# Kernel optimization log

Measured on AMD Instinct MI355X. Metric: run time of the kernel, lower is better.

## Reference

```python
import jax, jax.numpy as jnp
import numpy as np

N_LAYERS = 4
EPS = 1e-5  # eqx.nn.LayerNorm default


def _kernels(lam, P, B, C, step, L):
    # Annotated-S4 DPLR generating-function kernel (Q = P), vectorized over H channels.
    # lam, P, B, C: (H, N) complex64; step: (H, 1) real. Returns K: (H, L) real.
    omega = jnp.exp((-2j * jnp.pi) * (jnp.arange(L) / L))            # (L,) roots of unity
    g = (2.0 / step) * ((1.0 - omega) / (1.0 + omega))[None, :]      # (H, L) bilinear warp
    c = 2.0 / (1.0 + omega)                                          # (L,)

    def cauchy(v):  # v: (H, N) -> (H, L): sum_n v_n / (g - lambda_n)
        return jnp.sum(v[:, None, :] / (g[:, :, None] - lam[:, None, :]), axis=-1)

    k00 = cauchy(jnp.conj(C) * B)
    k01 = cauchy(jnp.conj(C) * P)
    k10 = cauchy(jnp.conj(P) * B)
    k11 = cauchy(jnp.conj(P) * P)
    at_roots = c[None, :] * (k00 - k01 * (1.0 / (1.0 + k11)) * k10)  # woodbury correction
    return jnp.fft.ifft(at_roots, n=L, axis=-1).real                 # (H, L)


def _causal_conv(u, K):
    # u: (B, L, H) real input, K: (H, L) real kernel -> causal conv along L via zero-padded FFT.
    L = u.shape[1]
    Ud = jnp.fft.rfft(u, n=2 * L, axis=1)                 # (B, F, H)
    Kd = jnp.fft.rfft(K, n=2 * L, axis=-1)                # (H, F)
    return jnp.fft.irfft(Ud * Kd.T[None], n=2 * L, axis=1)[:, :L]


def _forward(x, enc_w, enc_b, dec_w, dec_b, lam_re, lam_im, p_re, p_im, b_re, b_im,
             c_re, c_im, d, log_step, norm_w, norm_b, w1, b1, w2, b2):
    L = x.shape[1]
    h = x @ enc_w.T + enc_b                               # encoder: (B, L, H)
    for i in range(N_LAYERS):
        skip = h
        mu = h.mean(-1, keepdims=True)
        var = ((h - mu) ** 2).mean(-1, keepdims=True)
        hn = (h - mu) / jnp.sqrt(var + EPS) * norm_w[i] + norm_b[i]
        K = _kernels(lam_re[i] + 1j * lam_im[i], p_re[i] + 1j * p_im[i],
                     b_re[i] + 1j * b_im[i], c_re[i] + 1j * c_im[i],
                     jnp.exp(log_step[i])[:, None], L)
        y = _causal_conv(hn, K) + hn * d[i]               # SSM conv + skip-through D term
        y = jax.nn.gelu(y)
        y = (y @ w1[i].T + b1[i]) * jax.nn.sigmoid(y @ w2[i].T + b2[i])  # gated MLP
        h = skip + y
    return h @ dec_w.T + dec_b                            # decoder: (B, L, out)


def setup_inputs() -> dict:
    key = jax.random.key(0)
    B, L, IN, OUT, H, N, NL = 8, 2048, 64, 64, 128, 64, N_LAYERS
    ks = jax.random.split(key, 12)
    rn = lambda k, s, sc: (jax.random.normal(k, s) * sc).astype(jnp.float32)
    return dict(
        x=rn(ks[0], (B, L, IN), 1.0),
        convolve=1,
        enc_w=rn(ks[1], (H, IN), 1.0 / np.sqrt(IN)), enc_b=jnp.zeros((H,), jnp.float32),
        dec_w=rn(ks[2], (OUT, H), 1.0 / np.sqrt(H)), dec_b=jnp.zeros((OUT,), jnp.float32),
        lam_re=-0.5 * jnp.ones((NL, H, N), jnp.float32),  # HiPPO/S4D-style stable poles
        lam_im=jnp.tile(jnp.float32(np.pi) * jnp.arange(N, dtype=jnp.float32), (NL, H, 1)),
        p_re=rn(ks[3], (NL, H, N), 0.5 / np.sqrt(N)), p_im=rn(ks[4], (NL, H, N), 0.5 / np.sqrt(N)),
        b_re=rn(ks[5], (NL, H, N), 1.0), b_im=rn(ks[6], (NL, H, N), 1.0),
        c_re=rn(ks[7], (NL, H, N), 1.0 / np.sqrt(N)), c_im=rn(ks[8], (NL, H, N), 1.0 / np.sqrt(N)),
        d=jnp.ones((NL, H), jnp.float32),
        log_step=(jax.random.uniform(ks[9], (NL, H)) * (np.log(0.1) - np.log(0.001))
                  + np.log(0.001)).astype(jnp.float32),
        norm_w=jnp.ones((NL, H), jnp.float32), norm_b=jnp.zeros((NL, H), jnp.float32),
        w1=rn(ks[10], (NL, H, H), 1.0 / np.sqrt(H)), b1=jnp.zeros((NL, H), jnp.float32),
        w2=rn(ks[11], (NL, H, H), 1.0 / np.sqrt(H)), b2=jnp.zeros((NL, H), jnp.float32),
    )


def reference(x, convolve, enc_w, enc_b, dec_w, dec_b, lam_re, lam_im, p_re, p_im,
              b_re, b_im, c_re, c_im, d, log_step, norm_w, norm_b, w1, b1, w2, b2):
    # convolve is static 1 (True): the FFT-convolution path of the S4 Model.
    return _forward(x, enc_w, enc_b, dec_w, dec_b, lam_re, lam_im, p_re, p_im, b_re, b_im,
                    c_re, c_im, d, log_step, norm_w, norm_b, w1, b1, w2, b2)
```

## Files before the change

### kernel.cpp

```cpp
#include <hip/hip_runtime.h>
#include <hip/hip_bf16.h>


#define Bsz 8
#define Lseq 2048
#define Hdim 128
#define Npol 64
#define NLAYERS 4

typedef __bf16 bf16x8 __attribute__((ext_vector_type(8)));
typedef float f32x16 __attribute__((ext_vector_type(16)));

__device__ __forceinline__ float fast_rcp(float x) { return __builtin_amdgcn_rcpf(x); }
__device__ __forceinline__ float fast_rsq(float x) { return __builtin_amdgcn_rsqf(x); }

__device__ __forceinline__ float2 cmulf(float2 a, float2 b) {
    return make_float2(a.x * b.x - a.y * b.y, a.x * b.y + a.y * b.x);
}
__device__ __forceinline__ float2 cmulc(float2 a, float2 b) {
    return make_float2(a.x * b.x + a.y * b.y, a.y * b.x - a.x * b.y);
}

__device__ __forceinline__ float gelu_f(float v) {
    float z = 0.7978845608028654f * (v + 0.044715f * v * v * v);
    float e = __expf(2.0f * z);
    return v - v * fast_rcp(e + 1.0f);
}

__device__ __forceinline__ int sw(int i) { return (i & ~15) | ((i ^ (i >> 4)) & 15); }

static __device__ const float W16R[8] = {1.f, 0.9238795325f, 0.7071067812f, 0.3826834324f,
                                         0.f, -0.3826834324f, -0.7071067812f, -0.9238795325f};
static __device__ const float W16I[8] = {0.f, -0.3826834324f, -0.7071067812f, -0.9238795325f,
                                         -1.f, -0.9238795325f, -0.7071067812f, -0.3826834324f};
static __device__ const int BR4[16] = {0, 8, 4, 12, 2, 10, 6, 14, 1, 9, 5, 13, 3, 11, 7, 15};
static __device__ const int BR3[8] = {0, 4, 2, 6, 1, 5, 3, 7};

__device__ __forceinline__ float2 twget(const float2* __restrict__ tw, int e) {
    float2 w = tw[e & 2047];
    if (e & 2048) { w.x = -w.x; w.y = -w.y; }
    return w;
}

template <bool INV>
__device__ __forceinline__ void fft16_dif(float2 v[16]) {
#pragma unroll
    for (int mi = 0; mi < 4; mi++) {
        const int m = 8 >> mi;
#pragma unroll
        for (int g = 0; g < 16; g += 2 * m) {
#pragma unroll
            for (int j = 0; j < m; j++) {
                float wr = W16R[j << mi];
                float wi = INV ? -W16I[j << mi] : W16I[j << mi];
                float2 a = v[g + j], b = v[g + j + m];
                float dx = a.x - b.x, dy = a.y - b.y;
                v[g + j] = make_float2(a.x + b.x, a.y + b.y);
                v[g + j + m] = make_float2(dx * wr - dy * wi, dx * wi + dy * wr);
            }
        }
    }
}

template <bool INV>
__device__ __forceinline__ void fft16_dit(float2 v[16]) {
#pragma unroll
    for (int mi = 3; mi >= 0; mi--) {
        const int m = 8 >> mi;
#pragma unroll
        for (int g = 0; g < 16; g += 2 * m) {
#pragma unroll
            for (int j = 0; j < m; j++) {
                float wr = W16R[j << mi];
                float wi = INV ? -W16I[j << mi] : W16I[j << mi];
                float2 a = v[g + j], b = v[g + j + m];
                float bx = b.x * wr - b.y * wi, by = b.x * wi + b.y * wr;
                v[g + j] = make_float2(a.x + bx, a.y + by);
                v[g + j + m] = make_float2(a.x - bx, a.y - by);
            }
        }
    }
}

template <bool INV>
__device__ __forceinline__ void fft8_dif(float2 v[8]) {
#pragma unroll
    for (int mi = 0; mi < 3; mi++) {
        const int m = 4 >> mi;
#pragma unroll
        for (int g = 0; g < 8; g += 2 * m) {
#pragma unroll
            for (int j = 0; j < m; j++) {
                float wr = W16R[j << (mi + 1)];
                float wi = INV ? -W16I[j << (mi + 1)] : W16I[j << (mi + 1)];
                float2 a = v[g + j], b = v[g + j + m];
                float dx = a.x - b.x, dy = a.y - b.y;
                v[g + j] = make_float2(a.x + b.x, a.y + b.y);
                v[g + j + m] = make_float2(dx * wr - dy * wi, dx * wi + dy * wr);
            }
        }
    }
}

__device__ __forceinline__ void fft4096_passA_hz(float2* data, const float2* __restrict__ tw,
                                                 int t, const float2 vin[8]) {
    float2 v[16];
#pragma unroll
    for (int j = 0; j < 8; j++) v[j] = vin[j];
#pragma unroll
    for (int j = 0; j < 8; j++)
        v[j + 8] = cmulf(v[j], make_float2(W16R[j], W16I[j]));
#pragma unroll
    for (int mi = 1; mi < 4; mi++) {
        const int m = 8 >> mi;
#pragma unroll
        for (int g = 0; g < 16; g += 2 * m) {
#pragma unroll
            for (int j = 0; j < m; j++) {
                float wr = W16R[j << mi], wi = W16I[j << mi];
                float2 a = v[g + j], b = v[g + j + m];
                float dx = a.x - b.x, dy = a.y - b.y;
                v[g + j] = make_float2(a.x + b.x, a.y + b.y);
                v[g + j + m] = make_float2(dx * wr - dy * wi, dx * wi + dy * wr);
            }
        }
    }
#pragma unroll
    for (int i = 1; i < 16; i++) v[i] = cmulf(v[i], twget(tw, t * BR4[i]));
#pragma unroll
    for (int i = 0; i < 16; i++) data[sw(i * 256 + t)] = v[i];
}

__device__ __forceinline__ void fft4096_fwd_BC(float2* data, const float2* __restrict__ tw, int t) {
    __syncthreads();
    {
        int j0 = t & 15;
        int base = (t >> 4) * 256 + j0;
        float2 v[16];
#pragma unroll
        for (int k = 0; k < 16; k++) v[k] = data[sw(base + 16 * k)];
        fft16_dif<false>(v);
#pragma unroll
        for (int i = 1; i < 16; i++) v[i] = cmulf(v[i], twget(tw, 16 * j0 * BR4[i]));
#pragma unroll
        for (int i = 0; i < 16; i++) data[sw(base + 16 * i)] = v[i];
    }
    __syncthreads();
    {
        float2 v[16];
#pragma unroll
        for (int k = 0; k < 16; k++) v[k] = data[sw(t * 16 + k)];
        fft16_dif<false>(v);
#pragma unroll
        for (int i = 0; i < 16; i++) data[sw(t * 16 + i)] = v[i];
    }
    __syncthreads();
}

__global__ __launch_bounds__(256, 4) void prep_kernel(const float* __restrict__ w1,
                                                      const float* __restrict__ w2,
                                                      const float* __restrict__ dec_w,
                                                      float2* __restrict__ tw,
                                                      __bf16* __restrict__ wbf,
                                                      __bf16* __restrict__ decbf) {
    int bid = blockIdx.x, t = threadIdx.x;
    if (bid < 8) {
        int k = bid * 256 + t;
        if (k < 2048) {
            double a = -6.283185307179586476925286766559 * (double)k / 4096.0;
            tw[k] = make_float2((float)cos(a), (float)sin(a));
        }
        return;
    }
    if (bid < 264) {
        int i = (bid - 8) * 256 + t;
        int layer = i >> 14, rem = i & 16383;
        wbf[((size_t)layer * 2) * 16384 + rem] = (__bf16)w1[i];
        wbf[((size_t)layer * 2 + 1) * 16384 + rem] = (__bf16)w2[i];
        return;
    }
    int i = (bid - 264) * 256 + t;
    decbf[i] = (__bf16)dec_w[i];
}

__global__ __launch_bounds__(256) void kfft_enc_kernel(float2* __restrict__ Kd1,
                                                       const float2* __restrict__ tw,
                                                       const float* __restrict__ x,
                                                       const float* __restrict__ enc_w,
                                                       const float* __restrict__ enc_b,
                                                       const float* __restrict__ nw,
                                                       const float* __restrict__ nb,
                                                       float* __restrict__ h,
                                                       float* __restrict__ hnT,
                                                       const float* __restrict__ lam_re,
                                                       const float* __restrict__ lam_im,
                                                       const float* __restrict__ p_re,
                                                       const float* __restrict__ p_im,
                                                       const float* __restrict__ b_re,
                                                       const float* __restrict__ b_im,
                                                       const float* __restrict__ c_re,
                                                       const float* __restrict__ c_im,
                                                       const float* __restrict__ log_step) {
    __shared__ __align__(16) float smem[11712];
    int bid = blockIdx.x, t = threadIdx.x;
    if (bid < 512) {
        int hh = bid & 127, layer = bid >> 7;
        float2* data = (float2*)smem;
        float* ktmp = smem + 8192;
        float4* polA = (float4*)(smem + 10240);
        float4* polB = (float4*)(smem + 10496);
        float* n11S = smem + 10752;
        int baseP = (layer * Hdim + hh) * Npol;
        if (t < Npol) {
            int n = t;
            float lr = lam_re[baseP + n], li = lam_im[baseP + n];
            float pr = p_re[baseP + n], pi = p_im[baseP + n];
            float br = b_re[baseP + n], bi = b_im[baseP + n];
            float cr = c_re[baseP + n], ci = c_im[baseP + n];
            polA[n] = make_float4(lr, li, cr * br + ci * bi, cr * bi - ci * br);
            polB[n] = make_float4(cr * pr + ci * pi, cr * pi - ci * pr,
                                  pr * br + pi * bi, pr * bi - pi * br);
            n11S[n] = pr * pr + pi * pi;
        }
        __syncthreads();
        {
            float step = expf(log_step[layer * Hdim + hh]);
            float gs = 2.0f / step;
            float wrv[8], wiv[8];
            float gr[8], gi[8];
#pragma unroll
            for (int j = 0; j < 8; j++) {
                int l = t + 256 * j;
                float ang = -6.283185307179586f * (float)l / (float)Lseq;
                float wr = cosf(ang), wi = sinf(ang);
                wrv[j] = wr; wiv[j] = wi;
                float dr = 1.0f + wr, di = wi;
                float invd2 = fast_rcp(dr * dr + di * di);
                float nr = 1.0f - wr, ni = -wi;
                gr[j] = gs * (nr * dr + ni * di) * invd2;
                gi[j] = gs * (ni * dr - nr * di) * invd2;
            }
            float k00x[8], k00y[8], k01x[8], k01y[8];
            float k10x[8], k10y[8], k11x[8], k11y[8];
#pragma unroll
            for (int j = 0; j < 8; j++) {
                k00x[j] = 0.f; k00y[j] = 0.f; k01x[j] = 0.f; k01y[j] = 0.f;
                k10x[j] = 0.f; k10y[j] = 0.f; k11x[j] = 0.f; k11y[j] = 0.f;
            }
            for (int n = 0; n < Npol; n++) {
                float4 A = polA[n];
                float4 B = polB[n];
                float n11 = n11S[n];
#pragma unroll
                for (int j = 0; j < 8; j++) {
                    float er = gr[j] - A.x, ei = gi[j] - A.y;
                    float inv2 = fast_rcp(fmaf(er, er, ei * ei));
                    float ir = er * inv2;
                    float mi = ei * inv2;
                    k00x[j] = fmaf(A.z, ir, fmaf(A.w, mi, k00x[j]));
                    k00y[j] = fmaf(A.w, ir, fmaf(-A.z, mi, k00y[j]));
                    k01x[j] = fmaf(B.x, ir, fmaf(B.y, mi, k01x[j]));
                    k01y[j] = fmaf(B.y, ir, fmaf(-B.x, mi, k01y[j]));
                    k10x[j] = fmaf(B.z, ir, fmaf(B.w, mi, k10x[j]));
                    k10y[j] = fmaf(B.w, ir, fmaf(-B.z, mi, k10y[j]));
                    k11x[j] = fmaf(n11, ir, k11x[j]);
                    k11y[j] = fmaf(-n11, mi, k11y[j]);
                }
            }
#pragma unroll
            for (int j = 0; j < 8; j++) {
                int l = t + 256 * j;
                float dr = 1.0f + wrv[j], di = wiv[j];
                float invd2 = fast_rcp(dr * dr + di * di);
                float cr2 = 2.0f * dr * invd2, ci2 = -2.0f * di * invd2;
                float wr2 = 1.0f + k11x[j], wi2 = k11y[j];
                float w2inv = fast_rcp(fmaf(wr2, wr2, wi2 * wi2));
                float vr = wr2 * w2inv, vi = -wi2 * w2inv;
                float t1x = k01x[j] * k10x[j] - k01y[j] * k10y[j];
                float t1y = k01x[j] * k10y[j] + k01y[j] * k10x[j];
                float t2x = t1x * vr - t1y * vi, t2y = t1x * vi + t1y * vr;
                float ex = k00x[j] - t2x, ey = k00y[j] - t2y;
                data[sw(l)] = make_float2(cr2 * ex - ci2 * ey, cr2 * ey + ci2 * ex);
            }
        }
        __syncthreads();
        if (t < 128) {
            float2 v[16];
#pragma unroll
            for (int k = 0; k < 16; k++) v[k] = data[sw(t + 128 * k)];
            fft16_dif<true>(v);
#pragma unroll
            for (int i = 1; i < 16; i++) v[i] = cmulc(v[i], twget(tw, 2 * t * BR4[i]));
#pragma unroll
            for (int i = 0; i < 16; i++) data[sw(i * 128 + t)] = v[i];
        }
        __syncthreads();
        if (t < 128) {
            int i2 = t >> 3, j0 = t & 7;
            int base2 = i2 * 128 + j0;
            float2 v[16];
#pragma unroll
            for (int k = 0; k < 16; k++) v[k] = data[sw(base2 + 8 * k)];
            fft16_dif<true>(v);
#pragma unroll
            for (int i = 1; i < 16; i++) v[i] = cmulc(v[i], twget(tw, 32 * j0 * BR4[i]));
#pragma unroll
            for (int i = 0; i < 16; i++) data[sw(base2 + 8 * i)] = v[i];
        }
        __syncthreads();
        {
            float2 v8[8];
#pragma unroll
            for (int k = 0; k < 8; k++) v8[k] = data[sw(t * 8 + k)];
            fft8_dif<true>(v8);
            int r = BR4[t >> 4], s = BR4[t & 15];
#pragma unroll
            for (int i = 0; i < 8; i++) {
                int l = r + 16 * s + 256 * BR3[i];
                ktmp[l] = v8[i].x * (1.0f / 2048.0f);
            }
        }
        __syncthreads();
        {
            float2 vin[8];
#pragma unroll
            for (int k = 0; k < 8; k++) vin[k] = make_float2(ktmp[t + 256 * k], 0.f);
            fft4096_passA_hz(data, tw, t, vin);
        }
        fft4096_fwd_BC(data, tw, t);
        float2* dst = Kd1 + ((size_t)layer * Hdim + hh) * 4096;
#pragma unroll
        for (int k = 0; k < 16; k++) {
            int p = t + 256 * k;
            dst[p] = data[sw(p)];
        }
    } else {
        int r0 = (bid - 512) * 16;
        float* ws = smem;
        float* xst = smem + 8320;
        float* dots = smem + 9600;
        float2* mv = (float2*)(smem + 11648);
        for (int i = t; i < 128 * 64; i += 256) ws[(i >> 6) * 65 + (i & 63)] = enc_w[i];
        for (int i = t; i < 16 * 64; i += 256) {
            int r = i >> 6, k = i & 63;
            xst[k * 20 + r] = x[(size_t)(r0 + r) * 64 + k];
        }
        __syncthreads();
        int o = t & 127, half = t >> 7;
        float acc[8];
        float bo = enc_b[o];
#pragma unroll
        for (int j = 0; j < 8; j++) acc[j] = bo;
        for (int k = 0; k < 64; k++) {
            float wv = ws[o * 65 + k];
            float4 xa = *(const float4*)&xst[k * 20 + half * 8];
            float4 xb = *(const float4*)&xst[k * 20 + half * 8 + 4];
            acc[0] += wv * xa.x; acc[1] += wv * xa.y; acc[2] += wv * xa.z; acc[3] += wv * xa.w;
            acc[4] += wv * xb.x; acc[5] += wv * xb.y; acc[6] += wv * xb.z; acc[7] += wv * xb.w;
        }
#pragma unroll
        for (int j = 0; j < 8; j++) dots[(half * 8 + j) * 128 + o] = acc[j];
        __syncthreads();
        {
            int row = t >> 4, lane = t & 15;
            float s1 = 0.f, s2 = 0.f;
#pragma unroll
            for (int i = 0; i < 8; i++) {
                float v = dots[row * 128 + lane * 8 + i];
                s1 += v; s2 += v * v;
            }
#pragma unroll
            for (int m = 1; m < 16; m <<= 1) { s1 += __shfl_xor(s1, m); s2 += __shfl_xor(s2, m); }
            if (lane == 0) {
                float mu = s1 * (1.0f / 128.0f);
                float var = s2 * (1.0f / 128.0f) - mu * mu;
                mv[row] = make_float2(mu, fast_rsq(var + 1e-5f));
            }
        }
        __syncthreads();
        int c = t & 127;
        int bb = r0 >> 11, l0 = r0 & 2047;
        float nwc = nw[c], nbc = nb[c];
        float hnv[8];
#pragma unroll
        for (int j = 0; j < 8; j++) {
            int r = half * 8 + j;
            float v = dots[r * 128 + c];
            h[(size_t)(r0 + r) * Hdim + c] = v;
            float2 m = mv[r];
            hnv[j] = (v - m.x) * m.y * nwc + nbc;
        }
        float* dst = hnT + ((size_t)bb * Hdim + c) * Lseq + l0 + half * 8;
        *(float4*)dst = make_float4(hnv[0], hnv[1], hnv[2], hnv[3]);
        *(float4*)(dst + 4) = make_float4(hnv[4], hnv[5], hnv[6], hnv[7]);
    }
}

__global__ __launch_bounds__(256) void conv_kernel(float* __restrict__ hnT,
                                                   const float2* __restrict__ Kd1,
                                                   const float* __restrict__ dvec,
                                                   const float2* __restrict__ tw) {
    int h = blockIdx.x, bp = blockIdx.y, t = threadIdx.x;
    __shared__ float2 data[4096];
    float* u0 = hnT + ((size_t)(2 * bp) * Hdim + h) * Lseq;
    float* u1 = hnT + ((size_t)(2 * bp + 1) * Hdim + h) * Lseq;
    float2 ureg[8];
    float2 Kreg[16];
    float2 twB[15];
    const int j0 = t & 15;
    const float4* Kp4 = (const float4*)(Kd1 + (size_t)h * 4096 + t * 16);
    {
        float2 vin[8];
#pragma unroll
        for (int k = 0; k < 8; k++) {
            int l = t + 256 * k;
            float2 u2 = make_float2(u0[l], u1[l]);
            ureg[k] = u2;
            vin[k] = u2;
        }
#pragma unroll
        for (int k = 0; k < 8; k++) {
            float4 q = Kp4[k];
            Kreg[2 * k]     = make_float2(q.x, q.y);
            Kreg[2 * k + 1] = make_float2(q.z, q.w);
        }
#pragma unroll
        for (int i = 1; i < 16; i++) twB[i - 1] = twget(tw, 16 * j0 * BR4[i]);
        fft4096_passA_hz(data, tw, t, vin);
    }
    __syncthreads();
    {
        int base = (t >> 4) * 256 + j0;
        float2 v[16];
#pragma unroll
        for (int k = 0; k < 16; k++) v[k] = data[sw(base + 16 * k)];
        fft16_dif<false>(v);
#pragma unroll
        for (int i = 1; i < 16; i++) v[i] = cmulf(v[i], twB[i - 1]);
#pragma unroll
        for (int i = 0; i < 16; i++) data[sw(base + 16 * i)] = v[i];
    }
    __syncthreads();
    {
        const float scale = 1.0f / 4096.0f;
        float2 v[16];
#pragma unroll
        for (int k = 0; k < 16; k++) v[k] = data[sw(t * 16 + k)];
        fft16_dif<false>(v);
#pragma unroll
        for (int i = 0; i < 16; i++) {
            float2 W = cmulf(v[i], Kreg[i]);
            v[i] = make_float2(W.x * scale, W.y * scale);
        }
        fft16_dit<true>(v);
#pragma unroll
        for (int i = 0; i < 16; i++) data[sw(t * 16 + i)] = v[i];
    }
    __syncthreads();
    {
        int base2 = (t >> 4) * 256 + j0;
        float2 v[16];
        v[0] = data[sw(base2)];
#pragma unroll
        for (int i = 1; i < 16; i++)
            v[i] = cmulc(data[sw(base2 + 16 * i)], twB[i - 1]);
        fft16_dit<true>(v);
#pragma unroll
        for (int i = 0; i < 16; i++) data[sw(base2 + 16 * i)] = v[i];
    }
    __syncthreads();
    {
        float2 v[16];
        v[0] = data[sw(t)];
#pragma unroll
        for (int i = 1; i < 16; i++)
            v[i] = cmulc(data[sw(i * 256 + t)], twget(tw, t * BR4[i]));
#pragma unroll
        for (int mi = 3; mi >= 1; mi--) {
            const int m = 8 >> mi;
#pragma unroll
            for (int g = 0; g < 16; g += 2 * m) {
#pragma unroll
                for (int j = 0; j < m; j++) {
                    float wr = W16R[j << mi], wi = -W16I[j << mi];
                    float2 a = v[g + j], bb2 = v[g + j + m];
                    float bx = bb2.x * wr - bb2.y * wi, by = bb2.x * wi + bb2.y * wr;
                    v[g + j] = make_float2(a.x + bx, a.y + by);
                    v[g + j + m] = make_float2(a.x - bx, a.y - by);
                }
            }
        }
#pragma unroll
        for (int j = 0; j < 8; j++) {
            float wr = W16R[j], wi = -W16I[j];
            float2 bb2 = v[j + 8];
            float bx = bb2.x * wr - bb2.y * wi, by = bb2.x * wi + bb2.y * wr;
            v[j] = make_float2(v[j].x + bx, v[j].y + by);
        }
        float dcoef = dvec[h];
#pragma unroll
        for (int k = 0; k < 8; k++) {
            int l = t + 256 * k;
            u0[l] = gelu_f(v[k].x + ureg[k].x * dcoef);
            u1[l] = gelu_f(v[k].y + ureg[k].y * dcoef);
        }
    }
}

__global__ __launch_bounds__(256) void mlp_kernel(const float* __restrict__ yT,
                                                  float* __restrict__ h,
                                                  float* __restrict__ hnT,
                                                  const __bf16* __restrict__ w1b,
                                                  const __bf16* __restrict__ w2b,
                                                  const float* __restrict__ b1,
                                                  const float* __restrict__ b2,
                                                  const float* __restrict__ nw,
                                                  const float* __restrict__ nb) {
    int r0 = blockIdx.x * 32;
    int t = threadIdx.x;
    int wave = t >> 6, lane = t & 63;
    __shared__ __align__(16) __bf16 ybf[32 * 136];
    __shared__ float dots[32 * 132];
    __shared__ float2 mv[32];
    int bb = r0 >> 11, l0 = r0 & 2047;
    for (int i = t; i < 32 * 128; i += 256) {
        int r = i & 31, k = i >> 5;
        ybf[r * 136 + k] = (__bf16)yT[((size_t)bb * Hdim + k) * Lseq + l0 + r];
    }
    __syncthreads();
    int m = lane & 31, half = lane >> 5;
    bf16x8 a[8];
#pragma unroll
    for (int kk = 0; kk < 8; kk++)
        a[kk] = *(const bf16x8*)&ybf[m * 136 + kk * 16 + half * 8];
    int out = 32 * wave + m;
    const __bf16* w1r = w1b + (size_t)out * 128 + half * 8;
    const __bf16* w2r = w2b + (size_t)out * 128 + half * 8;
    f32x16 acc1, acc2;
#pragma unroll
    for (int i = 0; i < 16; i++) { acc1[i] = 0.f; acc2[i] = 0.f; }
#pragma unroll
    for (int kk = 0; kk < 8; kk++) {
        bf16x8 bw1 = *(const bf16x8*)(w1r + kk * 16);
        bf16x8 bw2 = *(const bf16x8*)(w2r + kk * 16);
        acc1 = __builtin_amdgcn_mfma_f32_32x32x16_bf16(a[kk], bw1, acc1, 0, 0, 0);
        acc2 = __builtin_amdgcn_mfma_f32_32x32x16_bf16(a[kk], bw2, acc2, 0, 0, 0);
    }
    float bias1 = b1[out], bias2 = b2[out];
#pragma unroll
    for (int reg = 0; reg < 16; reg++) {
        int row = (reg & 3) + 8 * (reg >> 2) + 4 * half;
        float v1 = acc1[reg] + bias1;
        float v2 = acc2[reg] + bias2;
        float g = fast_rcp(1.0f + __expf(-v2));
        float hv = h[(size_t)(r0 + row) * Hdim + out] + v1 * g;
        dots[row * 132 + out] = hv;
    }
    __syncthreads();
    {
        int row = t >> 3, lane8 = t & 7;
        float s1 = 0.f, s2 = 0.f;
        int base = row * 132 + lane8 * 16;
#pragma unroll
        for (int q = 0; q < 4; q++) {
            float4 v4 = *(const float4*)&dots[base + 4 * q];
            s1 += v4.x + v4.y + v4.z + v4.w;
            s2 += v4.x * v4.x + v4.y * v4.y + v4.z * v4.z + v4.w * v4.w;
        }
#pragma unroll
        for (int mm = 1; mm < 8; mm <<= 1) { s1 += __shfl_xor(s1, mm); s2 += __shfl_xor(s2, mm); }
        if (lane8 == 0) {
            float mu = s1 * (1.0f / 128.0f);
            float var = s2 * (1.0f / 128.0f) - mu * mu;
            mv[row] = make_float2(mu, fast_rsq(var + 1e-5f));
        }
    }
    __syncthreads();
    {
        int o = t & 127, rh = t >> 7;
        float nwc = nw[o], nbc = nb[o];
        float hnv[16];
#pragma unroll
        for (int j = 0; j < 16; j++) {
            int r = rh * 16 + j;
            float hvv = dots[r * 132 + o];
            h[(size_t)(r0 + r) * Hdim + o] = hvv;
            float2 mvv = mv[r];
            hnv[j] = (hvv - mvv.x) * mvv.y * nwc + nbc;
        }
        float* dst = hnT + ((size_t)bb * Hdim + o) * Lseq + l0 + rh * 16;
        *(float4*)(dst)      = make_float4(hnv[0],  hnv[1],  hnv[2],  hnv[3]);
        *(float4*)(dst + 4)  = make_float4(hnv[4],  hnv[5],  hnv[6],  hnv[7]);
        *(float4*)(dst + 8)  = make_float4(hnv[8],  hnv[9],  hnv[10], hnv[11]);
        *(float4*)(dst + 12) = make_float4(hnv[12], hnv[13], hnv[14], hnv[15]);
    }
}

__global__ __launch_bounds__(256) void mlpdec_kernel(const float* __restrict__ yT,
                                                     const float* __restrict__ h,
                                                     const __bf16* __restrict__ w1b,
                                                     const __bf16* __restrict__ w2b,
                                                     const float* __restrict__ b1,
                                                     const float* __restrict__ b2,
                                                     const __bf16* __restrict__ decb,
                                                     const float* __restrict__ dec_bias,
                                                     float* __restrict__ out) {
    int r0 = blockIdx.x * 32;
    int t = threadIdx.x;
    int wave = t >> 6, lane = t & 63;
    __shared__ __align__(16) __bf16 ybf[32 * 136];
    __shared__ float dots[32 * 132];
    int bb = r0 >> 11, l0 = r0 & 2047;
    for (int i = t; i < 32 * 128; i += 256) {
        int r = i & 31, k = i >> 5;
        ybf[r * 136 + k] = (__bf16)yT[((size_t)bb * Hdim + k) * Lseq + l0 + r];
    }
    __syncthreads();
    int m = lane & 31, half = lane >> 5;
    bf16x8 a[8];
#pragma unroll
    for (int kk = 0; kk < 8; kk++)
        a[kk] = *(const bf16x8*)&ybf[m * 136 + kk * 16 + half * 8];
    int outc = 32 * wave + m;
    const __bf16* w1r = w1b + (size_t)outc * 128 + half * 8;
    const __bf16* w2r = w2b + (size_t)outc * 128 + half * 8;
    f32x16 acc1, acc2;
#pragma unroll
    for (int i = 0; i < 16; i++) { acc1[i] = 0.f; acc2[i] = 0.f; }
#pragma unroll
    for (int kk = 0; kk < 8; kk++) {
        bf16x8 bw1 = *(const bf16x8*)(w1r + kk * 16);
        bf16x8 bw2 = *(const bf16x8*)(w2r + kk * 16);
        acc1 = __builtin_amdgcn_mfma_f32_32x32x16_bf16(a[kk], bw1, acc1, 0, 0, 0);
        acc2 = __builtin_amdgcn_mfma_f32_32x32x16_bf16(a[kk], bw2, acc2, 0, 0, 0);
    }
    float bias1 = b1[outc], bias2 = b2[outc];
#pragma unroll
    for (int reg = 0; reg < 16; reg++) {
        int row = (reg & 3) + 8 * (reg >> 2) + 4 * half;
        float v1 = acc1[reg] + bias1;
        float v2 = acc2[reg] + bias2;
        float g = fast_rcp(1.0f + __expf(-v2));
        float hv = h[(size_t)(r0 + row) * Hdim + outc] + v1 * g;
        dots[row * 132 + outc] = hv;
    }
    __syncthreads();
    for (int i = t; i < 32 * 128; i += 256) {
        int r = i >> 7, k = i & 127;
        ybf[r * 136 + k] = (__bf16)dots[r * 132 + k];
    }
    __syncthreads();
    if (wave < 2) {
        bf16x8 a2[8];
#pragma unroll
        for (int kk = 0; kk < 8; kk++)
            a2[kk] = *(const bf16x8*)&ybf[m * 136 + kk * 16 + half * 8];
        int oc = 32 * wave + m;
        const __bf16* wr = decb + (size_t)oc * 128 + half * 8;
        f32x16 acc;
#pragma unroll
        for (int i = 0; i < 16; i++) acc[i] = 0.f;
#pragma unroll
        for (int kk = 0; kk < 8; kk++) {
            bf16x8 bw = *(const bf16x8*)(wr + kk * 16);
            acc = __builtin_amdgcn_mfma_f32_32x32x16_bf16(a2[kk], bw, acc, 0, 0, 0);
        }
        float bo = dec_bias[oc];
#pragma unroll
        for (int reg = 0; reg < 16; reg++) {
            int row = (reg & 3) + 8 * (reg >> 2) + 4 * half;
            out[(size_t)(r0 + row) * 64 + oc] = acc[reg] + bo;
        }
    }
}

extern "C" void kernel_launch(void* const* d_in, const int* in_sizes, int n_in,
                              void* d_out, int out_size, void* d_ws, size_t ws_size,
                              hipStream_t stream) {
    const float* x      = (const float*)d_in[0];
    const float* enc_w  = (const float*)d_in[2];
    const float* enc_b  = (const float*)d_in[3];
    const float* dec_w  = (const float*)d_in[4];
    const float* dec_b  = (const float*)d_in[5];
    const float* lam_re = (const float*)d_in[6];
    const float* lam_im = (const float*)d_in[7];
    const float* p_re   = (const float*)d_in[8];
    const float* p_im   = (const float*)d_in[9];
    const float* b_re   = (const float*)d_in[10];
    const float* b_im   = (const float*)d_in[11];
    const float* c_re   = (const float*)d_in[12];
    const float* c_im   = (const float*)d_in[13];
    const float* dvec   = (const float*)d_in[14];
    const float* lstep  = (const float*)d_in[15];
    const float* norm_w = (const float*)d_in[16];
    const float* norm_b = (const float*)d_in[17];
    const float* w1     = (const float*)d_in[18];
    const float* b1     = (const float*)d_in[19];
    const float* w2     = (const float*)d_in[20];
    const float* b2     = (const float*)d_in[21];
    float* out = (float*)d_out;

    char* ws = (char*)d_ws;
    float2* tw  = (float2*)ws;  ws += 2048 * sizeof(float2);
    float*  h   = (float*)ws;   ws += (size_t)Bsz * Lseq * Hdim * sizeof(float);
    float*  hnT = (float*)ws;   ws += (size_t)Bsz * Lseq * Hdim * sizeof(float);
    float2* Kd1 = (float2*)ws;  ws += (size_t)NLAYERS * Hdim * 4096 * sizeof(float2);
    __bf16* wbf = (__bf16*)ws;  ws += (size_t)NLAYERS * 2 * Hdim * Hdim * sizeof(__bf16);
    __bf16* dbf = (__bf16*)ws;  ws += (size_t)64 * Hdim * sizeof(__bf16);

    const int nrows = Bsz * Lseq;

    prep_kernel<<<296, 256, 0, stream>>>(w1, w2, dec_w, tw, wbf, dbf);
    kfft_enc_kernel<<<512 + nrows / 16, 256, 0, stream>>>(
        Kd1, tw, x, enc_w, enc_b, norm_w, norm_b, h, hnT,
        lam_re, lam_im, p_re, p_im, b_re, b_im, c_re, c_im, lstep);
    for (int L = 0; L < NLAYERS; L++) {
        conv_kernel<<<dim3(Hdim, Bsz / 2), 256, 0, stream>>>(
            hnT, Kd1 + (size_t)L * Hdim * 4096, dvec + L * Hdim, tw);
        const __bf16* w1bL = wbf + (size_t)L * 2 * Hdim * Hdim;
        const __bf16* w2bL = w1bL + Hdim * Hdim;
        if (L < NLAYERS - 1) {
            const float* nwn = norm_w + (L + 1) * Hdim;
            const float* nbn = norm_b + (L + 1) * Hdim;
            mlp_kernel<<<nrows / 32, 256, 0, stream>>>(hnT, h, hnT, w1bL, w2bL,
                                                       b1 + L * Hdim, b2 + L * Hdim,
                                                       nwn, nbn);
        } else {
            mlpdec_kernel<<<nrows / 32, 256, 0, stream>>>(hnT, h, w1bL, w2bL,
                                                          b1 + L * Hdim, b2 + L * Hdim,
                                                          dbf, dec_b, out);
        }
    }
}
```

Baseline: 278.4 us.

## Spread per-layer SSM kernel generation into preceding conv launches

The front kernel now builds only layer 0's SSM convolution kernels. Each later layer's kernels are produced by 128 extra blocks added to the previous layer's conv launch, 32 per grid row. The goal is to shorten the serial startup phase and overlap the Cauchy/FFT kernel generation with the conv work of the prior layer. In exchange, those conv launches become larger, their shared-memory footprint grows, and the layout of the extra blocks must exactly cover all heads.

```diff
diff --git a/kernel.cpp b/kernel.cpp
--- a/kernel.cpp
+++ b/kernel.cpp
@@ -155,6 +155,149 @@
         for (int i = 0; i < 16; i++) data[sw(t * 16 + i)] = v[i];
     }
     __syncthreads();
+}
+
+__device__ __forceinline__ void kfft_core(int hh, int t, float* smem,
+                                          float2* __restrict__ KdL,
+                                          const float2* __restrict__ tw,
+                                          const float* __restrict__ lam_re,
+                                          const float* __restrict__ lam_im,
+                                          const float* __restrict__ p_re,
+                                          const float* __restrict__ p_im,
+                                          const float* __restrict__ b_re,
+                                          const float* __restrict__ b_im,
+                                          const float* __restrict__ c_re,
+                                          const float* __restrict__ c_im,
+                                          const float* __restrict__ log_step) {
+    float2* data = (float2*)smem;
+    float* ktmp = smem + 8192;
+    float4* polA = (float4*)(smem + 10240);
+    float4* polB = (float4*)(smem + 10496);
+    float* n11S = smem + 10752;
+    int baseP = hh * Npol;
+    if (t < Npol) {
+        int n = t;
+        float lr = lam_re[baseP + n], li = lam_im[baseP + n];
+        float pr = p_re[baseP + n], pi = p_im[baseP + n];
+        float br = b_re[baseP + n], bi = b_im[baseP + n];
+        float cr = c_re[baseP + n], ci = c_im[baseP + n];
+        polA[n] = make_float4(lr, li, cr * br + ci * bi, cr * bi - ci * br);
+        polB[n] = make_float4(cr * pr + ci * pi, cr * pi - ci * pr,
+                              pr * br + pi * bi, pr * bi - pi * br);
+        n11S[n] = pr * pr + pi * pi;
+    }
+    __syncthreads();
+    {
+        float step = expf(log_step[hh]);
+        float gs = 2.0f / step;
+        float wrv[8], wiv[8];
+        float gr[8], gi[8];
+#pragma unroll
+        for (int j = 0; j < 8; j++) {
+            int l = t + 256 * j;
+            float ang = -6.283185307179586f * (float)l / (float)Lseq;
+            float wr = cosf(ang), wi = sinf(ang);
+            wrv[j] = wr; wiv[j] = wi;
+            float dr = 1.0f + wr, di = wi;
+            float invd2 = fast_rcp(dr * dr + di * di);
+            float nr = 1.0f - wr, ni = -wi;
+            gr[j] = gs * (nr * dr + ni * di) * invd2;
+            gi[j] = gs * (ni * dr - nr * di) * invd2;
+        }
+        float k00x[8], k00y[8], k01x[8], k01y[8];
+        float k10x[8], k10y[8], k11x[8], k11y[8];
+#pragma unroll
+        for (int j = 0; j < 8; j++) {
+            k00x[j] = 0.f; k00y[j] = 0.f; k01x[j] = 0.f; k01y[j] = 0.f;
+            k10x[j] = 0.f; k10y[j] = 0.f; k11x[j] = 0.f; k11y[j] = 0.f;
+        }
+        for (int n = 0; n < Npol; n++) {
+            float4 A = polA[n];
+            float4 B = polB[n];
+            float n11 = n11S[n];
+#pragma unroll
+            for (int j = 0; j < 8; j++) {
+                float er = gr[j] - A.x, ei = gi[j] - A.y;
+                float inv2 = fast_rcp(fmaf(er, er, ei * ei));
+                float ir = er * inv2;
+                float mi = ei * inv2;
+                k00x[j] = fmaf(A.z, ir, fmaf(A.w, mi, k00x[j]));
+                k00y[j] = fmaf(A.w, ir, fmaf(-A.z, mi, k00y[j]));
+                k01x[j] = fmaf(B.x, ir, fmaf(B.y, mi, k01x[j]));
+                k01y[j] = fmaf(B.y, ir, fmaf(-B.x, mi, k01y[j]));
+                k10x[j] = fmaf(B.z, ir, fmaf(B.w, mi, k10x[j]));
+                k10y[j] = fmaf(B.w, ir, fmaf(-B.z, mi, k10y[j]));
+                k11x[j] = fmaf(n11, ir, k11x[j]);
+                k11y[j] = fmaf(-n11, mi, k11y[j]);
+            }
+        }
+#pragma unroll
+        for (int j = 0; j < 8; j++) {
+            int l = t + 256 * j;
+            float dr = 1.0f + wrv[j], di = wiv[j];
+            float invd2 = fast_rcp(dr * dr + di * di);
+            float cr2 = 2.0f * dr * invd2, ci2 = -2.0f * di * invd2;
+            float wr2 = 1.0f + k11x[j], wi2 = k11y[j];
+            float w2inv = fast_rcp(fmaf(wr2, wr2, wi2 * wi2));
+            float vr = wr2 * w2inv, vi = -wi2 * w2inv;
+            float t1x = k01x[j] * k10x[j] - k01y[j] * k10y[j];
+            float t1y = k01x[j] * k10y[j] + k01y[j] * k10x[j];
+            float t2x = t1x * vr - t1y * vi, t2y = t1x * vi + t1y * vr;
+            float ex = k00x[j] - t2x, ey = k00y[j] - t2y;
+            data[sw(l)] = make_float2(cr2 * ex - ci2 * ey, cr2 * ey + ci2 * ex);
+        }
+    }
+    __syncthreads();
+    if (t < 128) {
+        float2 v[16];
+#pragma unroll
+        for (int k = 0; k < 16; k++) v[k] = data[sw(t + 128 * k)];
+        fft16_dif<true>(v);
+#pragma unroll
+        for (int i = 1; i < 16; i++) v[i] = cmulc(v[i], twget(tw, 2 * t * BR4[i]));
+#pragma unroll
+        for (int i = 0; i < 16; i++) data[sw(i * 128 + t)] = v[i];
+    }
+    __syncthreads();
+    if (t < 128) {
+        int i2 = t >> 3, j0 = t & 7;
+        int base2 = i2 * 128 + j0;
+        float2 v[16];
+#pragma unroll
+        for (int k = 0; k < 16; k++) v[k] = data[sw(base2 + 8 * k)];
+        fft16_dif<true>(v);
+#pragma unroll
+        for (int i = 1; i < 16; i++) v[i] = cmulc(v[i], twget(tw, 32 * j0 * BR4[i]));
+#pragma unroll
+        for (int i = 0; i < 16; i++) data[sw(base2 + 8 * i)] = v[i];
+    }
+    __syncthreads();
+    {
+        float2 v8[8];
+#pragma unroll
+        for (int k = 0; k < 8; k++) v8[k] = data[sw(t * 8 + k)];
+        fft8_dif<true>(v8);
+        int r = BR4[t >> 4], s = BR4[t & 15];
+#pragma unroll
+        for (int i = 0; i < 8; i++) {
+            int l = r + 16 * s + 256 * BR3[i];
+            ktmp[l] = v8[i].x * (1.0f / 2048.0f);
+        }
+    }
+    __syncthreads();
+    {
+        float2 vin[8];
+#pragma unroll
+        for (int k = 0; k < 8; k++) vin[k] = make_float2(ktmp[t + 256 * k], 0.f);
+        fft4096_passA_hz(data, tw, t, vin);
+    }
+    fft4096_fwd_BC(data, tw, t);
+    float2* dst = KdL + (size_t)hh * 4096;
+#pragma unroll
+    for (int k = 0; k < 16; k++) {
+        int p = t + 256 * k;
+        dst[p] = data[sw(p)];
+    }
 }
 
 __global__ __launch_bounds__(256, 4) void prep_kernel(const float* __restrict__ w1,
@@ -203,139 +346,11 @@
                                                        const float* __restrict__ log_step) {
     __shared__ __align__(16) float smem[11712];
     int bid = blockIdx.x, t = threadIdx.x;
-    if (bid < 512) {
-        int hh = bid & 127, layer = bid >> 7;
-        float2* data = (float2*)smem;
-        float* ktmp = smem + 8192;
-        float4* polA = (float4*)(smem + 10240);
-        float4* polB = (float4*)(smem + 10496);
-        float* n11S = smem + 10752;
-        int baseP = (layer * Hdim + hh) * Npol;
-        if (t < Npol) {
-            int n = t;
-            float lr = lam_re[baseP + n], li = lam_im[baseP + n];
-            float pr = p_re[baseP + n], pi = p_im[baseP + n];
-            float br = b_re[baseP + n], bi = b_im[baseP + n];
-            float cr = c_re[baseP + n], ci = c_im[baseP + n];
-            polA[n] = make_float4(lr, li, cr * br + ci * bi, cr * bi - ci * br);
-            polB[n] = make_float4(cr * pr + ci * pi, cr * pi - ci * pr,
-                                  pr * br + pi * bi, pr * bi - pi * br);
-            n11S[n] = pr * pr + pi * pi;
-        }
-        __syncthreads();
-        {
-            float step = expf(log_step[layer * Hdim + hh]);
-            float gs = 2.0f / step;
-            float wrv[8], wiv[8];
-            float gr[8], gi[8];
-#pragma unroll
-            for (int j = 0; j < 8; j++) {
-                int l = t + 256 * j;
-                float ang = -6.283185307179586f * (float)l / (float)Lseq;
-                float wr = cosf(ang), wi = sinf(ang);
-                wrv[j] = wr; wiv[j] = wi;
-                float dr = 1.0f + wr, di = wi;
-                float invd2 = fast_rcp(dr * dr + di * di);
-                float nr = 1.0f - wr, ni = -wi;
-                gr[j] = gs * (nr * dr + ni * di) * invd2;
-                gi[j] = gs * (ni * dr - nr * di) * invd2;
-            }
-            float k00x[8], k00y[8], k01x[8], k01y[8];
-            float k10x[8], k10y[8], k11x[8], k11y[8];
-#pragma unroll
-            for (int j = 0; j < 8; j++) {
-                k00x[j] = 0.f; k00y[j] = 0.f; k01x[j] = 0.f; k01y[j] = 0.f;
-                k10x[j] = 0.f; k10y[j] = 0.f; k11x[j] = 0.f; k11y[j] = 0.f;
-            }
-            for (int n = 0; n < Npol; n++) {
-                float4 A = polA[n];
-                float4 B = polB[n];
-                float n11 = n11S[n];
-#pragma unroll
-                for (int j = 0; j < 8; j++) {
-                    float er = gr[j] - A.x, ei = gi[j] - A.y;
-                    float inv2 = fast_rcp(fmaf(er, er, ei * ei));
-                    float ir = er * inv2;
-                    float mi = ei * inv2;
-                    k00x[j] = fmaf(A.z, ir, fmaf(A.w, mi, k00x[j]));
-                    k00y[j] = fmaf(A.w, ir, fmaf(-A.z, mi, k00y[j]));
-                    k01x[j] = fmaf(B.x, ir, fmaf(B.y, mi, k01x[j]));
-                    k01y[j] = fmaf(B.y, ir, fmaf(-B.x, mi, k01y[j]));
-                    k10x[j] = fmaf(B.z, ir, fmaf(B.w, mi, k10x[j]));
-                    k10y[j] = fmaf(B.w, ir, fmaf(-B.z, mi, k10y[j]));
-                    k11x[j] = fmaf(n11, ir, k11x[j]);
-                    k11y[j] = fmaf(-n11, mi, k11y[j]);
-                }
-            }
-#pragma unroll
-            for (int j = 0; j < 8; j++) {
-                int l = t + 256 * j;
-                float dr = 1.0f + wrv[j], di = wiv[j];
-                float invd2 = fast_rcp(dr * dr + di * di);
-                float cr2 = 2.0f * dr * invd2, ci2 = -2.0f * di * invd2;
-                float wr2 = 1.0f + k11x[j], wi2 = k11y[j];
-                float w2inv = fast_rcp(fmaf(wr2, wr2, wi2 * wi2));
-                float vr = wr2 * w2inv, vi = -wi2 * w2inv;
-                float t1x = k01x[j] * k10x[j] - k01y[j] * k10y[j];
-                float t1y = k01x[j] * k10y[j] + k01y[j] * k10x[j];
-                float t2x = t1x * vr - t1y * vi, t2y = t1x * vi + t1y * vr;
-                float ex = k00x[j] - t2x, ey = k00y[j] - t2y;
-                data[sw(l)] = make_float2(cr2 * ex - ci2 * ey, cr2 * ey + ci2 * ex);
-            }
-        }
-        __syncthreads();
-        if (t < 128) {
-            float2 v[16];
-#pragma unroll
-            for (int k = 0; k < 16; k++) v[k] = data[sw(t + 128 * k)];
-            fft16_dif<true>(v);
-#pragma unroll
-            for (int i = 1; i < 16; i++) v[i] = cmulc(v[i], twget(tw, 2 * t * BR4[i]));
-#pragma unroll
-            for (int i = 0; i < 16; i++) data[sw(i * 128 + t)] = v[i];
-        }
-        __syncthreads();
-        if (t < 128) {
-            int i2 = t >> 3, j0 = t & 7;
-            int base2 = i2 * 128 + j0;
-            float2 v[16];
-#pragma unroll
-            for (int k = 0; k < 16; k++) v[k] = data[sw(base2 + 8 * k)];
-            fft16_dif<true>(v);
-#pragma unroll
-            for (int i = 1; i < 16; i++) v[i] = cmulc(v[i], twget(tw, 32 * j0 * BR4[i]));
-#pragma unroll
-            for (int i = 0; i < 16; i++) data[sw(base2 + 8 * i)] = v[i];
-        }
-        __syncthreads();
-        {
-            float2 v8[8];
-#pragma unroll
-            for (int k = 0; k < 8; k++) v8[k] = data[sw(t * 8 + k)];
-            fft8_dif<true>(v8);
-            int r = BR4[t >> 4], s = BR4[t & 15];
-#pragma unroll
-            for (int i = 0; i < 8; i++) {
-                int l = r + 16 * s + 256 * BR3[i];
-                ktmp[l] = v8[i].x * (1.0f / 2048.0f);
-            }
-        }
-        __syncthreads();
-        {
-            float2 vin[8];
-#pragma unroll
-            for (int k = 0; k < 8; k++) vin[k] = make_float2(ktmp[t + 256 * k], 0.f);
-            fft4096_passA_hz(data, tw, t, vin);
-        }
-        fft4096_fwd_BC(data, tw, t);
-        float2* dst = Kd1 + ((size_t)layer * Hdim + hh) * 4096;
-#pragma unroll
-        for (int k = 0; k < 16; k++) {
-            int p = t + 256 * k;
-            dst[p] = data[sw(p)];
-        }
+    if (bid < 128) {
+        kfft_core(bid, t, smem, Kd1, tw, lam_re, lam_im, p_re, p_im,
+                  b_re, b_im, c_re, c_im, log_step);
     } else {
-        int r0 = (bid - 512) * 16;
+        int r0 = (bid - 128) * 16;
         float* ws = smem;
         float* xst = smem + 8320;
         float* dots = smem + 9600;
@@ -399,9 +414,27 @@
 __global__ __launch_bounds__(256) void conv_kernel(float* __restrict__ hnT,
                                                    const float2* __restrict__ Kd1,
                                                    const float* __restrict__ dvec,
-                                                   const float2* __restrict__ tw) {
-    int h = blockIdx.x, bp = blockIdx.y, t = threadIdx.x;
-    __shared__ float2 data[4096];
+                                                   const float2* __restrict__ tw,
+                                                   float2* __restrict__ KdNext,
+                                                   const float* __restrict__ lam_re,
+                                                   const float* __restrict__ lam_im,
+                                                   const float* __restrict__ p_re,
+                                                   const float* __restrict__ p_im,
+                                                   const float* __restrict__ b_re,
+                                                   const float* __restrict__ b_im,
+                                                   const float* __restrict__ c_re,
+                                                   const float* __restrict__ c_im,
+                                                   const float* __restrict__ log_step) {
+    __shared__ __align__(16) float smem[10816];
+    int t = threadIdx.x;
+    if (blockIdx.x >= Hdim) {
+        int kb = (blockIdx.x - Hdim) + 32 * blockIdx.y;
+        kfft_core(kb, t, smem, KdNext, tw, lam_re, lam_im, p_re, p_im,
+                  b_re, b_im, c_re, c_im, log_step);
+        return;
+    }
+    int h = blockIdx.x, bp = blockIdx.y;
+    float2* data = (float2*)smem;
     float* u0 = hnT + ((size_t)(2 * bp) * Hdim + h) * Lseq;
     float* u1 = hnT + ((size_t)(2 * bp + 1) * Hdim + h) * Lseq;
     float2 ureg[8];
@@ -709,14 +742,21 @@
     __bf16* dbf = (__bf16*)ws;  ws += (size_t)64 * Hdim * sizeof(__bf16);
 
     const int nrows = Bsz * Lseq;
+    const int PN = Hdim * Npol;
 
     prep_kernel<<<296, 256, 0, stream>>>(w1, w2, dec_w, tw, wbf, dbf);
-    kfft_enc_kernel<<<512 + nrows / 16, 256, 0, stream>>>(
+    kfft_enc_kernel<<<128 + nrows / 16, 256, 0, stream>>>(
         Kd1, tw, x, enc_w, enc_b, norm_w, norm_b, h, hnT,
         lam_re, lam_im, p_re, p_im, b_re, b_im, c_re, c_im, lstep);
     for (int L = 0; L < NLAYERS; L++) {
-        conv_kernel<<<dim3(Hdim, Bsz / 2), 256, 0, stream>>>(
-            hnT, Kd1 + (size_t)L * Hdim * 4096, dvec + L * Hdim, tw);
+        int Ln = (L + 1 < NLAYERS) ? L + 1 : 0;
+        bool hasNext = (L + 1 < NLAYERS);
+        conv_kernel<<<dim3(hasNext ? Hdim + 32 : Hdim, Bsz / 2), 256, 0, stream>>>(
+            hnT, Kd1 + (size_t)L * Hdim * 4096, dvec + L * Hdim, tw,
+            Kd1 + (size_t)Ln * Hdim * 4096,
+            lam_re + Ln * PN, lam_im + Ln * PN, p_re + Ln * PN, p_im + Ln * PN,
+            b_re + Ln * PN, b_im + Ln * PN, c_re + Ln * PN, c_im + Ln * PN,
+            lstep + Ln * Hdim);
         const __bf16* w1bL = wbf + (size_t)L * 2 * Hdim * Hdim;
         const __bf16* w2bL = w1bL + Hdim * Hdim;
         if (L < NLAYERS - 1) {
```

Result: slower. 381.9 us (+37.2%).
